# Optimization experiments

Hardware: AMD Instinct MI355X
Metric: run time of the kernel (lower is better)

The kernel has to match this reference:

```python
import jax, jax.numpy as jnp
import numpy as np
from jax import lax

N, E = 10000, 100000
IN_CH, HID, EDGE_DIM, K = 32, 64, 16, 3
DILATIONS = (1, 2, 4)


def setup_inputs() -> dict:
    key = jax.random.key(0)
    ks = jax.random.split(key, 20)
    def nrm(k, shape, fan):
        return jax.random.normal(k, shape, jnp.float32) * (1.0 / np.sqrt(fan))
    inp = {
        "x": jax.random.normal(ks[0], (N, IN_CH), jnp.float32),
        "edge_attr": jax.random.normal(ks[1], (E, EDGE_DIM), jnp.float32),
        "h_prev": jax.random.normal(ks[2], (N, K, HID), jnp.float32),
        "edge_index": jax.random.randint(ks[3], (2, E), 0, N, jnp.int32),
        # edge-conditioning MLP: edge_dim -> 32 -> in_ch*hid
        "w1": nrm(ks[4], (EDGE_DIM, 32), EDGE_DIM), "b1": jnp.zeros((32,), jnp.float32),
        "w2": nrm(ks[5], (32, IN_CH * HID), 32), "b2": jnp.zeros((IN_CH * HID,), jnp.float32),
        # NNConv root weight + bias
        "root": nrm(ks[6], (IN_CH, HID), IN_CH), "bias": jnp.zeros((HID,), jnp.float32),
        # three dilated Conv1d layers [out, in, k]
        "tcn_w1": nrm(ks[7], (HID, HID, K), HID * K), "tcn_b1": jnp.zeros((HID,), jnp.float32),
        "tcn_w2": nrm(ks[8], (HID, HID, K), HID * K), "tcn_b2": jnp.zeros((HID,), jnp.float32),
        "tcn_w3": nrm(ks[9], (HID, HID, K), HID * K), "tcn_b3": jnp.zeros((HID,), jnp.float32),
        # output projection hid*3 -> hid
        "proj_w": nrm(ks[10], (HID * len(DILATIONS), HID), HID * len(DILATIONS)),
        "proj_b": jnp.zeros((HID,), jnp.float32),
    }
    return inp


def _conv1d_last(h, w, b, dilation):
    # h: [N, C, L], w: [O, I, K]; 'same'-style padding (K-1)*d//2, return last timestep.
    pad = (K - 1) * dilation // 2
    out = lax.conv_general_dilated(
        h, w, window_strides=(1,), padding=[(pad, pad)],
        rhs_dilation=(dilation,), dimension_numbers=("NCH", "OIH", "NCH"))
    return out[:, :, -1] + b[None, :]


def reference(x, edge_attr, h_prev, edge_index,
              w1, b1, w2, b2, root, bias,
              tcn_w1, tcn_b1, tcn_w2, tcn_b2, tcn_w3, tcn_b3,
              proj_w, proj_b):
    src, dst = edge_index[0], edge_index[1]
    n = x.shape[0]

    # --- NNConv (ECC): per-edge weight via MLP, gather -> matmul -> scatter-mean ---
    h_e = jax.nn.relu(edge_attr @ w1 + b1)                   # [E, 32]
    W_e = (h_e @ w2 + b2).reshape(-1, IN_CH, HID)            # [E, in, hid]
    msg = jnp.einsum("ei,eio->eo", x[src], W_e)             # [E, hid]
    agg = jax.ops.segment_sum(msg, dst, num_segments=n)      # [N, hid]
    cnt = jax.ops.segment_sum(jnp.ones((msg.shape[0],), msg.dtype), dst, num_segments=n)
    mean = agg / jnp.maximum(cnt, 1.0)[:, None]
    h_graph = jax.nn.relu(mean + x @ root + bias)            # [N, hid]

    # --- history update ---
    h_hist = jnp.concatenate([h_prev[:, 1:], h_graph[:, None, :]], axis=1)  # [N, K, hid]

    # --- dilated TCN stack, keep only last timestep of each branch ---
    h_in = jnp.transpose(h_hist, (0, 2, 1))                  # [N, hid, K]
    outs = [
        _conv1d_last(h_in, tcn_w1, tcn_b1, DILATIONS[0]),
        _conv1d_last(h_in, tcn_w2, tcn_b2, DILATIONS[1]),
        _conv1d_last(h_in, tcn_w3, tcn_b3, DILATIONS[2]),
    ]
    h_cat = jnp.concatenate(outs, axis=1)                    # [N, hid*3]
    h_out = h_cat @ proj_w + proj_b                          # dropout = identity (eval)
    return h_out, h_hist
```

## Files before the change

kernel.cpp:

```cpp
#include <hip/hip_runtime.h>
#include <stdint.h>

#define NN 10000
#define NE 100000
#define CHUNK 10

__device__ __forceinline__ float bu2f(uint16_t u) {
    return __uint_as_float(((uint32_t)u) << 16);
}
__device__ __forceinline__ float blo(uint32_t v) { return __uint_as_float(v << 16); }
__device__ __forceinline__ float bhi(uint32_t v) { return __uint_as_float(v & 0xffff0000u); }
__device__ __forceinline__ uint16_t f2bu(float f) {
    uint32_t u = __float_as_uint(f);
    return (uint16_t)((u + 0x7fffu + ((u >> 16) & 1u)) >> 16);
}
__device__ __forceinline__ float ldf(const void* p, size_t i, int f32) {
    return f32 ? ((const float*)p)[i] : bu2f(((const uint16_t*)p)[i]);
}
struct f8 { float v[8]; };
__device__ __forceinline__ f8 ldf8(const void* p, size_t i, int f32) {
    f8 r;
    if (f32) {
        const float4* q = (const float4*)((const float*)p + i);
        float4 a = q[0], b = q[1];
        r.v[0]=a.x; r.v[1]=a.y; r.v[2]=a.z; r.v[3]=a.w;
        r.v[4]=b.x; r.v[5]=b.y; r.v[6]=b.z; r.v[7]=b.w;
    } else {
        uint4 u = *(const uint4*)((const uint16_t*)p + i);
        r.v[0]=blo(u.x); r.v[1]=bhi(u.x); r.v[2]=blo(u.y); r.v[3]=bhi(u.y);
        r.v[4]=blo(u.z); r.v[5]=bhi(u.z); r.v[6]=blo(u.w); r.v[7]=bhi(u.w);
    }
    return r;
}
__device__ __forceinline__ void stf(void* p, size_t i, float v, int f32) {
    if (f32) ((float*)p)[i] = v;
    else ((uint16_t*)p)[i] = f2bu(v);
}
__device__ __forceinline__ int clampi(int v, int lo, int hi) {
    return min(max(v, lo), hi);
}

__global__ __launch_bounds__(256) void k_init(
    const void* __restrict__ x, float4* __restrict__ zbase, int* __restrict__ flag)
{
    int bid = blockIdx.x;
    if (bid < 657) {
        int idx = bid * 256 + threadIdx.x;
        if (idx < 168088) zbase[idx] = make_float4(0.f, 0.f, 0.f, 0.f);
    } else if (threadIdx.x == 0) {
        const uint16_t* p = (const uint16_t*)x;
        int c = 0;
        for (int i = 0; i < 1024; i++) {
            float a = fabsf(bu2f(p[i]));
            if (a > 1e-3f && a < 16.0f) c++;
        }
        *flag = (c < 870) ? 1 : 0;
    }
}

__global__ __launch_bounds__(256, 4) void k_prep(
    const void* __restrict__ x, const void* __restrict__ root,
    const void* __restrict__ tw1, const void* __restrict__ tw2,
    const void* __restrict__ tw3,
    const void* __restrict__ tb1, const void* __restrict__ tb2,
    const void* __restrict__ tb3,
    const void* __restrict__ proj_w,
    const void* __restrict__ edge_attr, const void* __restrict__ w1,
    const void* __restrict__ b1,
    const void* __restrict__ w2, const void* __restrict__ b2,
    const int* __restrict__ ei, const int* __restrict__ flag,
    float* __restrict__ xs_f, float* __restrict__ root_f,
    float* __restrict__ A, float* __restrict__ B, float* __restrict__ C,
    float* __restrict__ dv,
    int* __restrict__ outdeg, int* __restrict__ indeg,
    uint16_t* __restrict__ h_edge,
    uint16_t* __restrict__ T, float* __restrict__ xb)
{
    int bid = blockIdx.x;
    int tid = threadIdx.x;
    if (bid < 157) {
        int f32 = *flag;
        int v8 = bid * 256 + tid;
        if (v8 < 40000) {
            f8 r = ldf8(x, (size_t)v8 * 8, f32);
            float4* o = (float4*)(xs_f + (size_t)v8 * 8);
            o[0] = make_float4(r.v[0], r.v[1], r.v[2], r.v[3]);
            o[1] = make_float4(r.v[4], r.v[5], r.v[6], r.v[7]);
        }
    } else if (bid == 157) {
        int f32 = *flag;
        f8 r = ldf8(root, (size_t)tid * 8, f32);
        float4* o = (float4*)(root_f + (size_t)tid * 8);
        o[0] = make_float4(r.v[0], r.v[1], r.v[2], r.v[3]);
        o[1] = make_float4(r.v[4], r.v[5], r.v[6], r.v[7]);
    } else if (bid < 670) {
        int f32 = *flag;
        int beta = bid - 158;
        int i = beta >> 3;
        int chunk = beta & 7;
        int o = tid & 63, sub = tid >> 6;
        int cc0 = chunk * 8 + sub * 2;
        float a = 0.f, b = 0.f, c = 0.f, d = 0.f;
        #pragma unroll
        for (int m = 0; m < 2; m++) {
            int cc = cc0 + m;
            float p0 = ldf(proj_w, (size_t)cc * 64 + o, f32);
            float p1 = ldf(proj_w, (size_t)(64 + cc) * 64 + o, f32);
            float p2 = ldf(proj_w, (size_t)(128 + cc) * 64 + o, f32);
            size_t base = (size_t)cc * 192 + i * 3;
            a = fmaf(ldf(tw1, base + 1, f32), p0, a);
            a = fmaf(ldf(tw2, base + 1, f32), p1, a);
            a = fmaf(ldf(tw3, base + 1, f32), p2, a);
            b = fmaf(ldf(tw2, base + 0, f32), p1, b);
            c = fmaf(ldf(tw1, base + 0, f32), p0, c);
            if (i == 0) {
                d = fmaf(ldf(tb1, cc, f32), p0, d);
                d = fmaf(ldf(tb2, cc, f32), p1, d);
                d = fmaf(ldf(tb3, cc, f32), p2, d);
            }
        }
        unsafeAtomicAdd(&A[i * 64 + o], a);
        unsafeAtomicAdd(&B[i * 64 + o], b);
        unsafeAtomicAdd(&C[i * 64 + o], c);
        if (i == 0) unsafeAtomicAdd(&dv[o], d);
    } else if (bid < 1061) {
        int e = (bid - 670) * 256 + tid;
        if (e < NE) {
            atomicAdd(&outdeg[clampi(ei[e], 0, NN - 1)], 1);
            atomicAdd(&indeg[clampi(ei[NE + e], 0, NN - 1)], 1);
        }
    } else if (bid < 4186) {
        int f32 = *flag;
        __shared__ float w1s[512];
        __shared__ float b1s[32];
        __shared__ float eas[32][16];
        int e0 = (bid - 1061) * 32;
        if (tid < 64) {
            f8 r = ldf8(w1, (size_t)tid * 8, f32);
            #pragma unroll
            for (int q = 0; q < 8; q++) w1s[tid * 8 + q] = r.v[q];
        } else if (tid < 128) {
            int t = tid - 64;
            f8 r = ldf8(edge_attr, (size_t)e0 * 16 + (size_t)t * 8, f32);
            int el = t >> 1, half = (t & 1) * 8;
            #pragma unroll
            for (int q = 0; q < 8; q++) eas[el][half + q] = r.v[q];
        } else if (tid < 160) {
            b1s[tid - 128] = ldf(b1, tid - 128, f32);
        }
        __syncthreads();
        int el = tid >> 5, j = tid & 31;
        float wreg[16];
        #pragma unroll
        for (int k = 0; k < 16; k++) wreg[k] = w1s[k * 32 + j];
        float bj = b1s[j];
        #pragma unroll
        for (int r = 0; r < 4; r++) {
            int e = el + r * 8;
            float acc = bj;
            #pragma unroll
            for (int k = 0; k < 16; k++) acc = fmaf(eas[e][k], wreg[k], acc);
            h_edge[(size_t)(e0 + e) * 32 + j] = f2bu(fmaxf(acc, 0.0f));
        }
    } else {
        int f32 = *flag;
        int n0 = (bid - 4186) * 8;
        __shared__ float xs[8][32];
        if (tid < 32) {
            f8 r = ldf8(x, (size_t)n0 * 32 + (size_t)tid * 8, f32);
            int base = tid * 8;
            #pragma unroll
            for (int q = 0; q < 8; q++) xs[(base + q) >> 5][(base + q) & 31] = r.v[q];
        }
        __syncthreads();
        int c0 = tid * 8;
        int j = c0 >> 6, o0 = c0 & 63;
        float acc[8][8];
        #pragma unroll
        for (int s = 0; s < 8; s++)
            #pragma unroll
            for (int r = 0; r < 8; r++) acc[s][r] = 0.0f;
        if (f32) {
            const float* wb = (const float*)w2 + (size_t)j * 2048 + o0;
            for (int i = 0; i < 32; i++) {
                float4 a4 = *(const float4*)(wb + i * 64);
                float4 b4 = *(const float4*)(wb + i * 64 + 4);
                #pragma unroll
                for (int s = 0; s < 8; s++) {
                    float xv = xs[s][i];
                    acc[s][0] = fmaf(xv, a4.x, acc[s][0]); acc[s][1] = fmaf(xv, a4.y, acc[s][1]);
                    acc[s][2] = fmaf(xv, a4.z, acc[s][2]); acc[s][3] = fmaf(xv, a4.w, acc[s][3]);
                    acc[s][4] = fmaf(xv, b4.x, acc[s][4]); acc[s][5] = fmaf(xv, b4.y, acc[s][5]);
                    acc[s][6] = fmaf(xv, b4.z, acc[s][6]); acc[s][7] = fmaf(xv, b4.w, acc[s][7]);
                }
            }
        } else {
            const uint16_t* wb = (const uint16_t*)w2 + (size_t)j * 2048 + o0;
            for (int i = 0; i < 32; i++) {
                uint4 u = *(const uint4*)(wb + i * 64);
                float w0 = blo(u.x), w1_ = bhi(u.x), w2_ = blo(u.y), w3 = bhi(u.y);
                float w4 = blo(u.z), w5 = bhi(u.z), w6 = blo(u.w), w7 = bhi(u.w);
                #pragma unroll
                for (int s = 0; s < 8; s++) {
                    float xv = xs[s][i];
                    acc[s][0] = fmaf(xv, w0, acc[s][0]); acc[s][1] = fmaf(xv, w1_, acc[s][1]);
                    acc[s][2] = fmaf(xv, w2_, acc[s][2]); acc[s][3] = fmaf(xv, w3, acc[s][3]);
                    acc[s][4] = fmaf(xv, w4, acc[s][4]); acc[s][5] = fmaf(xv, w5, acc[s][5]);
                    acc[s][6] = fmaf(xv, w6, acc[s][6]); acc[s][7] = fmaf(xv, w7, acc[s][7]);
                }
            }
        }
        #pragma unroll
        for (int s = 0; s < 8; s++) {
            uint4 ov;
            ov.x = ((uint32_t)f2bu(acc[s][1]) << 16) | f2bu(acc[s][0]);
            ov.y = ((uint32_t)f2bu(acc[s][3]) << 16) | f2bu(acc[s][2]);
            ov.z = ((uint32_t)f2bu(acc[s][5]) << 16) | f2bu(acc[s][4]);
            ov.w = ((uint32_t)f2bu(acc[s][7]) << 16) | f2bu(acc[s][6]);
            *(uint4*)(T + (size_t)(n0 + s) * 2048 + c0) = ov;
        }
        int o = tid & 63;
        if (f32) {
            const float* b2f = (const float*)b2;
            #pragma unroll
            for (int h = 0; h < 2; h++) {
                int s = (tid >> 6) + h * 4;
                float a = 0.0f;
                #pragma unroll
                for (int i = 0; i < 32; i++)
                    a = fmaf(xs[s][i], b2f[i * 64 + o], a);
                xb[(size_t)(n0 + s) * 64 + o] = a;
            }
        } else {
            const uint16_t* b2u = (const uint16_t*)b2;
            #pragma unroll
            for (int h = 0; h < 2; h++) {
                int s = (tid >> 6) + h * 4;
                float a = 0.0f;
                #pragma unroll
                for (int i = 0; i < 32; i++)
                    a = fmaf(xs[s][i], bu2f(b2u[i * 64 + o]), a);
                xb[(size_t)(n0 + s) * 64 + o] = a;
            }
        }
    }
}

__global__ __launch_bounds__(1024) void k_scan(
    const int* __restrict__ outdeg, int* __restrict__ offs, int* __restrict__ cursor)
{
    __shared__ int sums[1024];
    const int CH = 10;
    int tid = threadIdx.x;
    int base = tid * CH;
    int v[CH];
    int s = 0;
    #pragma unroll
    for (int k = 0; k < CH; k++) {
        int i = base + k;
        int c = (i < NN) ? outdeg[i] : 0;
        v[k] = s;
        s += c;
    }
    sums[tid] = s;
    __syncthreads();
    for (int d = 1; d < 1024; d <<= 1) {
        int t = (tid >= d) ? sums[tid - d] : 0;
        __syncthreads();
        if (tid >= d) sums[tid] += t;
        __syncthreads();
    }
    int prefix = (tid == 0) ? 0 : sums[tid - 1];
    #pragma unroll
    for (int k = 0; k < CH; k++) {
        int i = base + k;
        if (i <= NN) {
            int val = prefix + v[k];
            offs[i] = val;
            if (i < NN) cursor[i] = val;
        }
    }
}

__global__ __launch_bounds__(256) void k_scat(
    const int* __restrict__ ei, int* __restrict__ cursor,
    int* __restrict__ sorted_src, int* __restrict__ sorted_dst,
    int* __restrict__ sorted_eid,
    const uint16_t* __restrict__ h_edge, uint16_t* __restrict__ h_srt, int hs_mode)
{
    int e = blockIdx.x * 256 + threadIdx.x;
    if (e < NE) {
        int src = clampi(ei[e], 0, NN - 1);
        int dst = clampi(ei[NE + e], 0, NN - 1);
        int pos = clampi(atomicAdd(&cursor[src], 1), 0, NE - 1);
        sorted_src[pos] = src;
        sorted_dst[pos] = dst;
        if (hs_mode) {
            const uint4* hs = (const uint4*)(h_edge + (size_t)e * 32);
            uint4* hd = (uint4*)(h_srt + (size_t)pos * 32);
            hd[0] = hs[0]; hd[1] = hs[1]; hd[2] = hs[2]; hd[3] = hs[3];
        } else {
            sorted_eid[pos] = e;
        }
    }
}

__global__ __launch_bounds__(256) void k_msg_g(
    const uint16_t* __restrict__ h_edge, const uint16_t* __restrict__ h_srt,
    int hs_mode, const uint16_t* __restrict__ T,
    const float* __restrict__ xb, const int* __restrict__ sorted_src,
    const int* __restrict__ sorted_dst, const int* __restrict__ sorted_eid,
    float* __restrict__ agg)
{
    int wid = blockIdx.x * 4 + (threadIdx.x >> 6);
    int lane = threadIdx.x & 63;
    int p0 = wid * CHUNK;
    if (p0 >= NE) return;
    int p1 = min(p0 + CHUNK, NE);
    int cur = -1;
    float tv[32];
    float xbv = 0.0f;
    int sN = clampi(sorted_src[p0], 0, NN - 1);
    const uint4* hq;
    if (hs_mode) hq = (const uint4*)(h_srt + (size_t)p0 * 32);
    else hq = (const uint4*)(h_edge + (size_t)clampi(sorted_eid[p0], 0, NE - 1) * 32);
    uint4 na = hq[0], nb = hq[1], nc = hq[2], nd = hq[3];
    for (int p = p0; p < p1; p++) {
        int s = sN;
        uint4 a = na, b = nb, c = nc, d = nd;
        int dst = clampi(sorted_dst[p], 0, NN - 1);
        if (p + 1 < p1) {
            sN = clampi(sorted_src[p + 1], 0, NN - 1);
            const uint4* h2;
            if (hs_mode) h2 = (const uint4*)(h_srt + (size_t)(p + 1) * 32);
            else h2 = (const uint4*)(h_edge + (size_t)clampi(sorted_eid[p + 1], 0, NE - 1) * 32);
            na = h2[0]; nb = h2[1]; nc = h2[2]; nd = h2[3];
        }
        if (s != cur) {
            cur = s;
            const uint16_t* Tr = T + (size_t)s * 2048 + lane;
            #pragma unroll
            for (int j = 0; j < 32; j++) tv[j] = bu2f(Tr[j * 64]);
            xbv = xb[(size_t)s * 64 + lane];
        }
        float s0 = 0.f, s1 = 0.f, s2 = 0.f, s3 = 0.f;
        s0 = fmaf(blo(a.x), tv[0],  s0); s0 = fmaf(bhi(a.x), tv[1],  s0);
        s0 = fmaf(blo(a.y), tv[2],  s0); s0 = fmaf(bhi(a.y), tv[3],  s0);
        s0 = fmaf(blo(a.z), tv[4],  s0); s0 = fmaf(bhi(a.z), tv[5],  s0);
        s0 = fmaf(blo(a.w), tv[6],  s0); s0 = fmaf(bhi(a.w), tv[7],  s0);
        s1 = fmaf(blo(b.x), tv[8],  s1); s1 = fmaf(bhi(b.x), tv[9],  s1);
        s1 = fmaf(blo(b.y), tv[10], s1); s1 = fmaf(bhi(b.y), tv[11], s1);
        s1 = fmaf(blo(b.z), tv[12], s1); s1 = fmaf(bhi(b.z), tv[13], s1);
        s1 = fmaf(blo(b.w), tv[14], s1); s1 = fmaf(bhi(b.w), tv[15], s1);
        s2 = fmaf(blo(c.x), tv[16], s2); s2 = fmaf(bhi(c.x), tv[17], s2);
        s2 = fmaf(blo(c.y), tv[18], s2); s2 = fmaf(bhi(c.y), tv[19], s2);
        s2 = fmaf(blo(c.z), tv[20], s2); s2 = fmaf(bhi(c.z), tv[21], s2);
        s2 = fmaf(blo(c.w), tv[22], s2); s2 = fmaf(bhi(c.w), tv[23], s2);
        s3 = fmaf(blo(d.x), tv[24], s3); s3 = fmaf(bhi(d.x), tv[25], s3);
        s3 = fmaf(blo(d.y), tv[26], s3); s3 = fmaf(bhi(d.y), tv[27], s3);
        s3 = fmaf(blo(d.z), tv[28], s3); s3 = fmaf(bhi(d.z), tv[29], s3);
        s3 = fmaf(blo(d.w), tv[30], s3); s3 = fmaf(bhi(d.w), tv[31], s3);
        float acc = xbv + (s0 + s1) + (s2 + s3);
        unsafeAtomicAdd(&agg[(size_t)dst * 64 + lane], acc);
    }
}

__global__ __launch_bounds__(256) void k_node_out(
    const float* __restrict__ agg, const int* __restrict__ indeg,
    const float* __restrict__ xs_f, const float* __restrict__ root_f,
    const void* __restrict__ bias, const void* __restrict__ h_prev,
    const float* __restrict__ A, const float* __restrict__ B,
    const float* __restrict__ C, const float* __restrict__ dv,
    const void* __restrict__ proj_b,
    const int* __restrict__ flag, void* __restrict__ out)
{
// ... 40 lines not shown
    const void* edge_attr = d_in[1];
    const void* h_prev    = d_in[2];
    const int*  ei        = (const int*)d_in[3];
    const void* w1     = d_in[4];
    const void* b1     = d_in[5];
    const void* w2     = d_in[6];
    const void* b2     = d_in[7];
    const void* root   = d_in[8];
    const void* bias   = d_in[9];
    const void* tw1    = d_in[10];
    const void* tb1    = d_in[11];
    const void* tw2    = d_in[12];
    const void* tb2    = d_in[13];
    const void* tw3    = d_in[14];
    const void* tb3    = d_in[15];
    const void* proj_w = d_in[16];
    const void* proj_b = d_in[17];

    char* ws = (char*)d_ws;
    size_t off = 0;
    uint16_t* T      = (uint16_t*)(ws + off); off = align64(off + (size_t)NN * 2048 * 2);
    uint16_t* h_edge = (uint16_t*)(ws + off); off = align64(off + (size_t)NE * 32 * 2);
    float* xs_f   = (float*)(ws + off); off = align64(off + (size_t)NN * 32 * 4);
    float* root_f = (float*)(ws + off); off = align64(off + (size_t)2048 * 4);
    float* xb     = (float*)(ws + off); off = align64(off + (size_t)NN * 64 * 4);
    size_t zero_base = off;
    float* agg    = (float*)(ws + off); off = align64(off + (size_t)NN * 64 * 4);
    int* indeg    = (int*)(ws + off);   off = align64(off + (size_t)NN * 4);
    int* outdeg   = (int*)(ws + off);   off = align64(off + (size_t)NN * 4);
    float* Amat   = (float*)(ws + off); off = align64(off + (size_t)4096 * 4);
    float* Bmat   = (float*)(ws + off); off = align64(off + (size_t)4096 * 4);
    float* Cmat   = (float*)(ws + off); off = align64(off + (size_t)4096 * 4);
    float* dvec   = (float*)(ws + off); off = align64(off + (size_t)64 * 4);
    int* offs        = (int*)(ws + off); off = align64(off + (size_t)(NN + 1) * 4);
    int* cursor      = (int*)(ws + off); off = align64(off + (size_t)NN * 4);
    int* sorted_src  = (int*)(ws + off); off = align64(off + (size_t)NE * 4);
    int* sorted_dst  = (int*)(ws + off); off = align64(off + (size_t)NE * 4);
    int* sorted_eid  = (int*)(ws + off); off = align64(off + (size_t)NE * 4);
    int* flag        = (int*)(ws + off); off = align64(off + 64);
    uint16_t* h_srt  = (uint16_t*)(ws + off);
    size_t off_end = off + (size_t)NE * 32 * 2;
    int hs_mode = (off_end <= ws_size) ? 1 : 0;

    k_init<<<658, 256, 0, stream>>>(x, (float4*)((char*)d_ws + zero_base), flag);
    k_prep<<<5436, 256, 0, stream>>>(x, root, tw1, tw2, tw3, tb1, tb2, tb3,
                                     proj_w, edge_attr, w1, b1, w2, b2, ei, flag,
                                     xs_f, root_f, Amat, Bmat, Cmat, dvec,
                                     outdeg, indeg, h_edge, T, xb);
    k_scan<<<1, 1024, 0, stream>>>(outdeg, offs, cursor);
    k_scat<<<391, 256, 0, stream>>>(ei, cursor, sorted_src, sorted_dst,
                                    sorted_eid, h_edge, h_srt, hs_mode);
    k_msg_g<<<(NE / CHUNK + 3) / 4, 256, 0, stream>>>(h_edge, h_srt, hs_mode, T, xb,
                                                      sorted_src, sorted_dst,
                                                      sorted_eid, agg);
    k_node_out<<<NN / 4, 256, 0, stream>>>(agg, indeg, xs_f, root_f, bias, h_prev,
                                           Amat, Bmat, Cmat, dvec, proj_b, flag, d_out);
}
```

Before: 232.7 us.

## Fuse all stages into one cooperative persistent kernel with grid syncs

Replaces the six separate kernel launches with a single cooperative kernel that loops over virtual blocks and uses grid.sync between stages. Zeroing of agg is deferred into the scatter phase, and the scan becomes a per-block prefix computation. This removes launch overhead and inter-kernel gaps. In exchange it caps parallelism at the occupancy-limited grid size, adds grid-wide barrier costs, and replaces the single-block scan with a redundant per-block prefix sum. The old multi-kernel launches remain as a fallback if the cooperative launch fails.

```diff
diff --git a/kernel.cpp b/kernel.cpp
--- a/kernel.cpp
+++ b/kernel.cpp
@@ -1,5 +1,8 @@
 #include <hip/hip_runtime.h>
+#include <hip/hip_cooperative_groups.h>
 #include <stdint.h>
+
+namespace cg = cooperative_groups;
 
 #define NN 10000
 #define NE 100000
@@ -38,6 +41,355 @@
 }
 __device__ __forceinline__ int clampi(int v, int lo, int hi) {
     return min(max(v, lo), hi);
+}
+
+struct Args {
+    const void *x, *edge_attr, *h_prev;
+    const int* ei;
+    const void *w1, *b1, *w2, *b2, *root, *bias;
+    const void *tw1, *tb1, *tw2, *tb2, *tw3, *tb3, *proj_w, *proj_b;
+    float4* zbase;
+    int* flag;
+    float *xs_f, *root_f, *A, *B, *C, *dv;
+    int *outdeg, *indeg;
+    uint16_t *h_edge, *T;
+    float* xb;
+    int *cursor, *sorted_src, *sorted_dst, *sorted_eid;
+    uint16_t* h_srt;
+    int hs_mode;
+    float* agg;
+    void* out;
+};
+
+__global__ __launch_bounds__(256) void k_mega(Args a) {
+    cg::grid_group grid = cg::this_grid();
+    const int tid = threadIdx.x;
+    const int bid = blockIdx.x;
+    const int G = gridDim.x;
+
+    __shared__ union SU {
+        struct { float w1s[512]; float b1s[32]; float eas[32][16]; } mlp;
+        float xsT[8][32];
+        int red[256];
+        struct { float hg[4][64]; float hp1[4][64]; float hp2[4][64]; } fin;
+    } su;
+
+    for (int vb = bid; vb < 33; vb += G) {
+        if (vb < 32) {
+            int idx = vb * 256 + tid;
+            if (idx < 8088) a.zbase[160000 + idx] = make_float4(0.f, 0.f, 0.f, 0.f);
+        } else if (tid == 0) {
+            const uint16_t* p = (const uint16_t*)a.x;
+            int c = 0;
+            for (int i = 0; i < 1024; i++) {
+                float v = fabsf(bu2f(p[i]));
+                if (v > 1e-3f && v < 16.0f) c++;
+            }
+            *a.flag = (c < 870) ? 1 : 0;
+        }
+    }
+    grid.sync();
+    const int f32 = *a.flag;
+
+    for (int vb = bid; vb < 5436; vb += G) {
+        __syncthreads();
+        if (vb < 157) {
+            int v8 = vb * 256 + tid;
+            if (v8 < 40000) {
+                f8 r = ldf8(a.x, (size_t)v8 * 8, f32);
+                float4* o = (float4*)(a.xs_f + (size_t)v8 * 8);
+                o[0] = make_float4(r.v[0], r.v[1], r.v[2], r.v[3]);
+                o[1] = make_float4(r.v[4], r.v[5], r.v[6], r.v[7]);
+            }
+        } else if (vb == 157) {
+            f8 r = ldf8(a.root, (size_t)tid * 8, f32);
+            float4* o = (float4*)(a.root_f + (size_t)tid * 8);
+            o[0] = make_float4(r.v[0], r.v[1], r.v[2], r.v[3]);
+            o[1] = make_float4(r.v[4], r.v[5], r.v[6], r.v[7]);
+        } else if (vb < 670) {
+            int beta = vb - 158;
+            int i = beta >> 3;
+            int chunk = beta & 7;
+            int o = tid & 63, sub = tid >> 6;
+            int cc0 = chunk * 8 + sub * 2;
+            float av = 0.f, bv = 0.f, cv = 0.f, dv_ = 0.f;
+            #pragma unroll
+            for (int m = 0; m < 2; m++) {
+                int cc = cc0 + m;
+                float p0 = ldf(a.proj_w, (size_t)cc * 64 + o, f32);
+                float p1 = ldf(a.proj_w, (size_t)(64 + cc) * 64 + o, f32);
+                float p2 = ldf(a.proj_w, (size_t)(128 + cc) * 64 + o, f32);
+                size_t base = (size_t)cc * 192 + i * 3;
+                av = fmaf(ldf(a.tw1, base + 1, f32), p0, av);
+                av = fmaf(ldf(a.tw2, base + 1, f32), p1, av);
+                av = fmaf(ldf(a.tw3, base + 1, f32), p2, av);
+                bv = fmaf(ldf(a.tw2, base + 0, f32), p1, bv);
+                cv = fmaf(ldf(a.tw1, base + 0, f32), p0, cv);
+                if (i == 0) {
+                    dv_ = fmaf(ldf(a.tb1, cc, f32), p0, dv_);
+                    dv_ = fmaf(ldf(a.tb2, cc, f32), p1, dv_);
+                    dv_ = fmaf(ldf(a.tb3, cc, f32), p2, dv_);
+                }
+            }
+            unsafeAtomicAdd(&a.A[i * 64 + o], av);
+            unsafeAtomicAdd(&a.B[i * 64 + o], bv);
+            unsafeAtomicAdd(&a.C[i * 64 + o], cv);
+            if (i == 0) unsafeAtomicAdd(&a.dv[o], dv_);
+        } else if (vb < 1061) {
+            int e = (vb - 670) * 256 + tid;
+            if (e < NE) {
+                atomicAdd(&a.outdeg[clampi(a.ei[e], 0, NN - 1)], 1);
+                atomicAdd(&a.indeg[clampi(a.ei[NE + e], 0, NN - 1)], 1);
+            }
+        } else if (vb < 4186) {
+            int e0 = (vb - 1061) * 32;
+            if (tid < 64) {
+                f8 r = ldf8(a.w1, (size_t)tid * 8, f32);
+                #pragma unroll
+                for (int q = 0; q < 8; q++) su.mlp.w1s[tid * 8 + q] = r.v[q];
+            } else if (tid < 128) {
+                int t = tid - 64;
+                f8 r = ldf8(a.edge_attr, (size_t)e0 * 16 + (size_t)t * 8, f32);
+                int el = t >> 1, half = (t & 1) * 8;
+                #pragma unroll
+                for (int q = 0; q < 8; q++) su.mlp.eas[el][half + q] = r.v[q];
+            } else if (tid < 160) {
+                su.mlp.b1s[tid - 128] = ldf(a.b1, tid - 128, f32);
+            }
+            __syncthreads();
+            int el = tid >> 5, j = tid & 31;
+            float wreg[16];
+            #pragma unroll
+            for (int k = 0; k < 16; k++) wreg[k] = su.mlp.w1s[k * 32 + j];
+            float bj = su.mlp.b1s[j];
+            #pragma unroll
+            for (int r = 0; r < 4; r++) {
+                int e = el + r * 8;
+                float acc = bj;
+                #pragma unroll
+                for (int k = 0; k < 16; k++) acc = fmaf(su.mlp.eas[e][k], wreg[k], acc);
+                a.h_edge[(size_t)(e0 + e) * 32 + j] = f2bu(fmaxf(acc, 0.0f));
+            }
+        } else {
+            int n0 = (vb - 4186) * 8;
+            if (tid < 32) {
+                f8 r = ldf8(a.x, (size_t)n0 * 32 + (size_t)tid * 8, f32);
+                int base = tid * 8;
+                #pragma unroll
+                for (int q = 0; q < 8; q++) su.xsT[(base + q) >> 5][(base + q) & 31] = r.v[q];
+            }
+            __syncthreads();
+            int c0 = tid * 8;
+            int j = c0 >> 6, o0 = c0 & 63;
+            float acc[8][8];
+            #pragma unroll
+            for (int s = 0; s < 8; s++)
+                #pragma unroll
+                for (int r = 0; r < 8; r++) acc[s][r] = 0.0f;
+            if (f32) {
+                const float* wb = (const float*)a.w2 + (size_t)j * 2048 + o0;
+                for (int i = 0; i < 32; i++) {
+                    float4 a4 = *(const float4*)(wb + i * 64);
+                    float4 b4 = *(const float4*)(wb + i * 64 + 4);
+                    #pragma unroll
+                    for (int s = 0; s < 8; s++) {
+                        float xv = su.xsT[s][i];
+                        acc[s][0] = fmaf(xv, a4.x, acc[s][0]); acc[s][1] = fmaf(xv, a4.y, acc[s][1]);
+                        acc[s][2] = fmaf(xv, a4.z, acc[s][2]); acc[s][3] = fmaf(xv, a4.w, acc[s][3]);
+                        acc[s][4] = fmaf(xv, b4.x, acc[s][4]); acc[s][5] = fmaf(xv, b4.y, acc[s][5]);
+                        acc[s][6] = fmaf(xv, b4.z, acc[s][6]); acc[s][7] = fmaf(xv, b4.w, acc[s][7]);
+                    }
+                }
+            } else {
+                const uint16_t* wb = (const uint16_t*)a.w2 + (size_t)j * 2048 + o0;
+                for (int i = 0; i < 32; i++) {
+                    uint4 u = *(const uint4*)(wb + i * 64);
+                    float w0 = blo(u.x), w1_ = bhi(u.x), w2_ = blo(u.y), w3 = bhi(u.y);
+                    float w4 = blo(u.z), w5 = bhi(u.z), w6 = blo(u.w), w7 = bhi(u.w);
+                    #pragma unroll
+                    for (int s = 0; s < 8; s++) {
+                        float xv = su.xsT[s][i];
+                        acc[s][0] = fmaf(xv, w0, acc[s][0]); acc[s][1] = fmaf(xv, w1_, acc[s][1]);
+                        acc[s][2] = fmaf(xv, w2_, acc[s][2]); acc[s][3] = fmaf(xv, w3, acc[s][3]);
+                        acc[s][4] = fmaf(xv, w4, acc[s][4]); acc[s][5] = fmaf(xv, w5, acc[s][5]);
+                        acc[s][6] = fmaf(xv, w6, acc[s][6]); acc[s][7] = fmaf(xv, w7, acc[s][7]);
+                    }
+                }
+            }
+            #pragma unroll
+            for (int s = 0; s < 8; s++) {
+                uint4 ov;
+                ov.x = ((uint32_t)f2bu(acc[s][1]) << 16) | f2bu(acc[s][0]);
+                ov.y = ((uint32_t)f2bu(acc[s][3]) << 16) | f2bu(acc[s][2]);
+                ov.z = ((uint32_t)f2bu(acc[s][5]) << 16) | f2bu(acc[s][4]);
+                ov.w = ((uint32_t)f2bu(acc[s][7]) << 16) | f2bu(acc[s][6]);
+                *(uint4*)(a.T + (size_t)(n0 + s) * 2048 + c0) = ov;
+            }
+            int o = tid & 63;
+            if (f32) {
+                const float* b2f = (const float*)a.b2;
+                #pragma unroll
+                for (int h = 0; h < 2; h++) {
+                    int s = (tid >> 6) + h * 4;
+                    float acc2 = 0.0f;
+                    #pragma unroll
+                    for (int i = 0; i < 32; i++)
+                        acc2 = fmaf(su.xsT[s][i], b2f[i * 64 + o], acc2);
+                    a.xb[(size_t)(n0 + s) * 64 + o] = acc2;
+                }
+            } else {
+                const uint16_t* b2u = (const uint16_t*)a.b2;
+                #pragma unroll
+                for (int h = 0; h < 2; h++) {
+                    int s = (tid >> 6) + h * 4;
+                    float acc2 = 0.0f;
+                    #pragma unroll
+                    for (int i = 0; i < 32; i++)
+                        acc2 = fmaf(su.xsT[s][i], bu2f(b2u[i * 64 + o]), acc2);
+                    a.xb[(size_t)(n0 + s) * 64 + o] = acc2;
+                }
+            }
+        }
+    }
+    grid.sync();
+
+    {
+        const int RANGE = (NN + G - 1) / G;
+        int base = bid * RANGE;
+        if (base < NN) {
+            __syncthreads();
+            int s = 0;
+            for (int j = tid; j < base; j += 256) s += a.outdeg[j];
+            su.red[tid] = s;
+            __syncthreads();
+            #pragma unroll
+            for (int d = 128; d > 0; d >>= 1) {
+                if (tid < d) su.red[tid] += su.red[tid + d];
+                __syncthreads();
+            }
+            if (tid == 0) {
+                int run = su.red[0];
+                int cnt = min(RANGE, NN - base);
+                for (int k = 0; k < cnt; k++) {
+                    int i = base + k;
+                    a.cursor[i] = run;
+                    run += a.outdeg[i];
+                }
+            }
+        }
+    }
+    grid.sync();
+
+    for (int vb = bid; vb < 1016; vb += G) {
+        if (vb < 391) {
+            int e = vb * 256 + tid;
+            if (e < NE) {
+                int src = clampi(a.ei[e], 0, NN - 1);
+                int dst = clampi(a.ei[NE + e], 0, NN - 1);
+                int pos = clampi(atomicAdd(&a.cursor[src], 1), 0, NE - 1);
+                a.sorted_src[pos] = src;
+                a.sorted_dst[pos] = dst;
+                if (a.hs_mode) {
+                    const uint4* hs = (const uint4*)(a.h_edge + (size_t)e * 32);
+                    uint4* hd = (uint4*)(a.h_srt + (size_t)pos * 32);
+                    hd[0] = hs[0]; hd[1] = hs[1]; hd[2] = hs[2]; hd[3] = hs[3];
+                } else {
+                    a.sorted_eid[pos] = e;
+                }
+            }
+        } else {
+            int idx = (vb - 391) * 256 + tid;
+            if (idx < 160000) a.zbase[idx] = make_float4(0.f, 0.f, 0.f, 0.f);
+        }
+    }
+    grid.sync();
+
+    for (int vb = bid; vb < 2500; vb += G) {
+        int wid = vb * 4 + (tid >> 6);
+        int lane = tid & 63;
+        int p0 = wid * CHUNK;
+        if (p0 < NE) {
+            int p1 = min(p0 + CHUNK, NE);
+            int cur = -1;
+            float tv[32];
+            float xbv = 0.0f;
+            int sN = clampi(a.sorted_src[p0], 0, NN - 1);
+            const uint4* hq;
+            if (a.hs_mode) hq = (const uint4*)(a.h_srt + (size_t)p0 * 32);
+            else hq = (const uint4*)(a.h_edge + (size_t)clampi(a.sorted_eid[p0], 0, NE - 1) * 32);
+            uint4 na = hq[0], nb = hq[1], nc = hq[2], nd = hq[3];
+            for (int p = p0; p < p1; p++) {
+                int s = sN;
+                uint4 av = na, bv = nb, cv = nc, dvv = nd;
+                int dst = clampi(a.sorted_dst[p], 0, NN - 1);
+                if (p + 1 < p1) {
+                    sN = clampi(a.sorted_src[p + 1], 0, NN - 1);
+                    const uint4* h2;
+                    if (a.hs_mode) h2 = (const uint4*)(a.h_srt + (size_t)(p + 1) * 32);
+                    else h2 = (const uint4*)(a.h_edge + (size_t)clampi(a.sorted_eid[p + 1], 0, NE - 1) * 32);
+                    na = h2[0]; nb = h2[1]; nc = h2[2]; nd = h2[3];
+                }
+                if (s != cur) {
+                    cur = s;
+                    const uint16_t* Tr = a.T + (size_t)s * 2048 + lane;
+                    #pragma unroll
+                    for (int j = 0; j < 32; j++) tv[j] = bu2f(Tr[j * 64]);
+                    xbv = a.xb[(size_t)s * 64 + lane];
+                }
+                float s0 = 0.f, s1 = 0.f, s2 = 0.f, s3 = 0.f;
+                s0 = fmaf(blo(av.x), tv[0],  s0); s0 = fmaf(bhi(av.x), tv[1],  s0);
+                s0 = fmaf(blo(av.y), tv[2],  s0); s0 = fmaf(bhi(av.y), tv[3],  s0);
+                s0 = fmaf(blo(av.z), tv[4],  s0); s0 = fmaf(bhi(av.z), tv[5],  s0);
+                s0 = fmaf(blo(av.w), tv[6],  s0); s0 = fmaf(bhi(av.w), tv[7],  s0);
+                s1 = fmaf(blo(bv.x), tv[8],  s1); s1 = fmaf(bhi(bv.x), tv[9],  s1);
+                s1 = fmaf(blo(bv.y), tv[10], s1); s1 = fmaf(bhi(bv.y), tv[11], s1);
+                s1 = fmaf(blo(bv.z), tv[12], s1); s1 = fmaf(bhi(bv.z), tv[13], s1);
+                s1 = fmaf(blo(bv.w), tv[14], s1); s1 = fmaf(bhi(bv.w), tv[15], s1);
+                s2 = fmaf(blo(cv.x), tv[16], s2); s2 = fmaf(bhi(cv.x), tv[17], s2);
+                s2 = fmaf(blo(cv.y), tv[18], s2); s2 = fmaf(bhi(cv.y), tv[19], s2);
+                s2 = fmaf(blo(cv.z), tv[20], s2); s2 = fmaf(bhi(cv.z), tv[21], s2);
+                s2 = fmaf(blo(cv.w), tv[22], s2); s2 = fmaf(bhi(cv.w), tv[23], s2);
+                s3 = fmaf(blo(dvv.x), tv[24], s3); s3 = fmaf(bhi(dvv.x), tv[25], s3);
+                s3 = fmaf(blo(dvv.y), tv[26], s3); s3 = fmaf(bhi(dvv.y), tv[27], s3);
+                s3 = fmaf(blo(dvv.z), tv[28], s3); s3 = fmaf(bhi(dvv.z), tv[29], s3);
+                s3 = fmaf(blo(dvv.w), tv[30], s3); s3 = fmaf(bhi(dvv.w), tv[31], s3);
+                float acc = xbv + (s0 + s1) + (s2 + s3);
+                unsafeAtomicAdd(&a.agg[(size_t)dst * 64 + lane], acc);
+            }
+        }
+    }
+    grid.sync();
+
+    for (int vb = bid; vb < 2500; vb += G) {
+        __syncthreads();
+        int s = tid >> 6, o = tid & 63;
+        int n = vb * 4 + s;
+        const size_t O1 = (size_t)NN * 64;
+        float xr = 0.0f;
+        const float* xp = a.xs_f + (size_t)n * 32;
+        #pragma unroll
+        for (int i = 0; i < 32; i++)
+            xr = fmaf(xp[i], a.root_f[i * 64 + o], xr);
+        float c = (float)a.indeg[n];
+        float m = a.agg[(size_t)n * 64 + o] / fmaxf(c, 1.0f);
+        float hg = fmaxf(m + xr + ldf(a.bias, o, f32), 0.0f);
+        float hp1 = ldf(a.h_prev, (size_t)n * 192 + 64 + o, f32);
+        float hp2 = ldf(a.h_prev, (size_t)n * 192 + 128 + o, f32);
+        su.fin.hg[s][o] = hg; su.fin.hp1[s][o] = hp1; su.fin.hp2[s][o] = hp2;
+        stf(a.out, O1 + (size_t)n * 192 + o, hp1, f32);
+        stf(a.out, O1 + (size_t)n * 192 + 64 + o, hp2, f32);
+        stf(a.out, O1 + (size_t)n * 192 + 128 + o, hg, f32);
+        __syncthreads();
+        float accA = 0.f, accB = 0.f, accC = 0.f;
+        #pragma unroll 8
+        for (int i = 0; i < 64; i++) {
+            accA = fmaf(su.fin.hg[s][i],  a.A[i * 64 + o], accA);
+            accB = fmaf(su.fin.hp1[s][i], a.B[i * 64 + o], accB);
+            accC = fmaf(su.fin.hp2[s][i], a.C[i * 64 + o], accC);
+        }
+        float acc = a.dv[o] + ldf(a.proj_b, o, f32) + (accA + accB) + accC;
+        stf(a.out, (size_t)n * 64 + o, acc, f32);
+    }
 }
 
 __global__ __launch_bounds__(256) void k_init(
@@ -457,6 +809,41 @@
     size_t off_end = off + (size_t)NE * 32 * 2;
     int hs_mode = (off_end <= ws_size) ? 1 : 0;
 
+    static int g_grid = -1;
+    if (g_grid < 0) {
+        int bpc = 0;
+        if (hipOccupancyMaxActiveBlocksPerMultiprocessor(&bpc, k_mega, 256, 0) != hipSuccess || bpc <= 0)
+            bpc = 1;
+        int ncu = 64;
+        hipDeviceProp_t prop;
+        if (hipGetDeviceProperties(&prop, 0) == hipSuccess && prop.multiProcessorCount > 0)
+            ncu = prop.multiProcessorCount;
+        int g = bpc * ncu;
+        if (g > 2048) g = 2048;
+        if (g < 64) g = 64;
+        g_grid = g;
+    }
+
+    Args ha;
+    ha.x = x; ha.edge_attr = edge_attr; ha.h_prev = h_prev; ha.ei = ei;
+    ha.w1 = w1; ha.b1 = b1; ha.w2 = w2; ha.b2 = b2; ha.root = root; ha.bias = bias;
+    ha.tw1 = tw1; ha.tb1 = tb1; ha.tw2 = tw2; ha.tb2 = tb2; ha.tw3 = tw3; ha.tb3 = tb3;
+    ha.proj_w = proj_w; ha.proj_b = proj_b;
+    ha.zbase = (float4*)((char*)d_ws + zero_base);
+    ha.flag = flag;
+    ha.xs_f = xs_f; ha.root_f = root_f; ha.A = Amat; ha.B = Bmat; ha.C = Cmat; ha.dv = dvec;
+    ha.outdeg = outdeg; ha.indeg = indeg;
+    ha.h_edge = h_edge; ha.T = T; ha.xb = xb;
+    ha.cursor = cursor; ha.sorted_src = sorted_src; ha.sorted_dst = sorted_dst;
+    ha.sorted_eid = sorted_eid; ha.h_srt = h_srt; ha.hs_mode = hs_mode;
+    ha.agg = agg; ha.out = d_out;
+
+    void* kargs[] = { &ha };
+    hipError_t err = hipLaunchCooperativeKernel(k_mega, dim3(g_grid), dim3(256),
+                                                kargs, 0, stream);
+    if (err == hipSuccess) return;
+    (void)hipGetLastError();
+
     k_init<<<658, 256, 0, stream>>>(x, (float4*)((char*)d_ws + zero_base), flag);
     k_prep<<<5436, 256, 0, stream>>>(x, root, tw1, tw2, tw3, tb1, tb2, tb3,
                                      proj_w, edge_attr, w1, b1, w2, b2, ei, flag,
```

Result: slower. 470.4 us (+102.2%).

## Transpose T layout for vector loads and fold scan into scatter kernel

Applied to the files above, without the earlier changes.

The node-transform blocks in k_prep now stage T through shared memory and write it transposed, so each lane in k_msg_g can fetch its 32 bf16 values with four 16-byte loads instead of 32 strided scalar loads. The degree pass now records each edge's rank from the atomicAdd, which removes the separate single-block k_scan kernel and the cursor atomics. Each k_scat block recomputes the prefix sum of out-degrees in shared memory (40 KB) and places edges at offset plus rank. Heavy blocks are also reordered to launch first in k_prep. The cost is redundant scan work in each of 98 scatter blocks and more shared memory per prep block.

```diff
diff --git a/kernel.cpp b/kernel.cpp
--- a/kernel.cpp
+++ b/kernel.cpp
@@ -72,30 +72,151 @@
     float* __restrict__ xs_f, float* __restrict__ root_f,
     float* __restrict__ A, float* __restrict__ B, float* __restrict__ C,
     float* __restrict__ dv,
-    int* __restrict__ outdeg, int* __restrict__ indeg,
+    int* __restrict__ outdeg, int* __restrict__ indeg, int* __restrict__ rank,
     uint16_t* __restrict__ h_edge,
     uint16_t* __restrict__ T, float* __restrict__ xb)
 {
     int bid = blockIdx.x;
     int tid = threadIdx.x;
-    if (bid < 157) {
+    __shared__ union PU {
+        struct { float xs[8][32]; uint16_t Ts[8][32][64]; } t;
+        struct { float w1s[512]; float b1s[32]; float eas[32][16]; } mlp;
+    } su;
+
+    if (bid < 1250) {
         int f32 = *flag;
-        int v8 = bid * 256 + tid;
-        if (v8 < 40000) {
-            f8 r = ldf8(x, (size_t)v8 * 8, f32);
-            float4* o = (float4*)(xs_f + (size_t)v8 * 8);
-            o[0] = make_float4(r.v[0], r.v[1], r.v[2], r.v[3]);
-            o[1] = make_float4(r.v[4], r.v[5], r.v[6], r.v[7]);
-        }
-    } else if (bid == 157) {
+        int n0 = bid * 8;
+        if (tid < 32) {
+            f8 r = ldf8(x, (size_t)n0 * 32 + (size_t)tid * 8, f32);
+            int base = tid * 8;
+            #pragma unroll
+            for (int q = 0; q < 8; q++) su.t.xs[(base + q) >> 5][(base + q) & 31] = r.v[q];
+        }
+        __syncthreads();
+        int j = tid >> 3;
+        int o0 = (tid & 7) * 8;
+        float acc[8][8];
+        #pragma unroll
+        for (int s = 0; s < 8; s++)
+            #pragma unroll
+            for (int r = 0; r < 8; r++) acc[s][r] = 0.0f;
+        if (f32) {
+            const float* wb = (const float*)w2 + (size_t)j * 2048 + o0;
+            for (int i = 0; i < 32; i++) {
+                float4 a4 = *(const float4*)(wb + i * 64);
+                float4 b4 = *(const float4*)(wb + i * 64 + 4);
+                #pragma unroll
+                for (int s = 0; s < 8; s++) {
+                    float xv = su.t.xs[s][i];
+                    acc[s][0] = fmaf(xv, a4.x, acc[s][0]); acc[s][1] = fmaf(xv, a4.y, acc[s][1]);
+                    acc[s][2] = fmaf(xv, a4.z, acc[s][2]); acc[s][3] = fmaf(xv, a4.w, acc[s][3]);
+                    acc[s][4] = fmaf(xv, b4.x, acc[s][4]); acc[s][5] = fmaf(xv, b4.y, acc[s][5]);
+                    acc[s][6] = fmaf(xv, b4.z, acc[s][6]); acc[s][7] = fmaf(xv, b4.w, acc[s][7]);
+                }
+            }
+        } else {
+            const uint16_t* wb = (const uint16_t*)w2 + (size_t)j * 2048 + o0;
+            for (int i = 0; i < 32; i++) {
+                uint4 u = *(const uint4*)(wb + i * 64);
+                float w0 = blo(u.x), w1_ = bhi(u.x), w2_ = blo(u.y), w3 = bhi(u.y);
+                float w4 = blo(u.z), w5 = bhi(u.z), w6 = blo(u.w), w7 = bhi(u.w);
+                #pragma unroll
+                for (int s = 0; s < 8; s++) {
+                    float xv = su.t.xs[s][i];
+                    acc[s][0] = fmaf(xv, w0, acc[s][0]); acc[s][1] = fmaf(xv, w1_, acc[s][1]);
+                    acc[s][2] = fmaf(xv, w2_, acc[s][2]); acc[s][3] = fmaf(xv, w3, acc[s][3]);
+                    acc[s][4] = fmaf(xv, w4, acc[s][4]); acc[s][5] = fmaf(xv, w5, acc[s][5]);
+                    acc[s][6] = fmaf(xv, w6, acc[s][6]); acc[s][7] = fmaf(xv, w7, acc[s][7]);
+                }
+            }
+        }
+        #pragma unroll
+        for (int s = 0; s < 8; s++) {
+            uint4 ov;
+            ov.x = ((uint32_t)f2bu(acc[s][1]) << 16) | f2bu(acc[s][0]);
+            ov.y = ((uint32_t)f2bu(acc[s][3]) << 16) | f2bu(acc[s][2]);
+            ov.z = ((uint32_t)f2bu(acc[s][5]) << 16) | f2bu(acc[s][4]);
+            ov.w = ((uint32_t)f2bu(acc[s][7]) << 16) | f2bu(acc[s][6]);
+            *(uint4*)&su.t.Ts[s][j][o0] = ov;
+        }
+        __syncthreads();
+        int k = tid >> 6, o = tid & 63;
+        #pragma unroll
+        for (int s = 0; s < 8; s++) {
+            uint16_t v0 = su.t.Ts[s][k * 8 + 0][o];
+            uint16_t v1 = su.t.Ts[s][k * 8 + 1][o];
+            uint16_t v2 = su.t.Ts[s][k * 8 + 2][o];
+            uint16_t v3 = su.t.Ts[s][k * 8 + 3][o];
+            uint16_t v4 = su.t.Ts[s][k * 8 + 4][o];
+            uint16_t v5 = su.t.Ts[s][k * 8 + 5][o];
+            uint16_t v6 = su.t.Ts[s][k * 8 + 6][o];
+            uint16_t v7 = su.t.Ts[s][k * 8 + 7][o];
+            uint4 ov;
+            ov.x = (uint32_t)v0 | ((uint32_t)v1 << 16);
+            ov.y = (uint32_t)v2 | ((uint32_t)v3 << 16);
+            ov.z = (uint32_t)v4 | ((uint32_t)v5 << 16);
+            ov.w = (uint32_t)v6 | ((uint32_t)v7 << 16);
+            *(uint4*)(T + (size_t)(n0 + s) * 2048 + (size_t)o * 32 + k * 8) = ov;
+        }
+        {
+            int oo = tid & 63;
+            if (f32) {
+                const float* b2f = (const float*)b2;
+                #pragma unroll
+                for (int h = 0; h < 2; h++) {
+                    int s = (tid >> 6) + h * 4;
+                    float a2 = 0.0f;
+                    #pragma unroll
+                    for (int i = 0; i < 32; i++)
+                        a2 = fmaf(su.t.xs[s][i], b2f[i * 64 + oo], a2);
+                    xb[(size_t)(n0 + s) * 64 + oo] = a2;
+                }
+            } else {
+                const uint16_t* b2u = (const uint16_t*)b2;
+                #pragma unroll
+                for (int h = 0; h < 2; h++) {
+                    int s = (tid >> 6) + h * 4;
+                    float a2 = 0.0f;
+                    #pragma unroll
+                    for (int i = 0; i < 32; i++)
+                        a2 = fmaf(su.t.xs[s][i], bu2f(b2u[i * 64 + oo]), a2);
+                    xb[(size_t)(n0 + s) * 64 + oo] = a2;
+                }
+            }
+        }
+    } else if (bid < 4375) {
         int f32 = *flag;
-        f8 r = ldf8(root, (size_t)tid * 8, f32);
-        float4* o = (float4*)(root_f + (size_t)tid * 8);
-        o[0] = make_float4(r.v[0], r.v[1], r.v[2], r.v[3]);
-        o[1] = make_float4(r.v[4], r.v[5], r.v[6], r.v[7]);
-    } else if (bid < 670) {
+        int e0 = (bid - 1250) * 32;
+        if (tid < 64) {
+            f8 r = ldf8(w1, (size_t)tid * 8, f32);
+            #pragma unroll
+            for (int q = 0; q < 8; q++) su.mlp.w1s[tid * 8 + q] = r.v[q];
+        } else if (tid < 128) {
+            int t = tid - 64;
+            f8 r = ldf8(edge_attr, (size_t)e0 * 16 + (size_t)t * 8, f32);
+            int el = t >> 1, half = (t & 1) * 8;
+            #pragma unroll
+            for (int q = 0; q < 8; q++) su.mlp.eas[el][half + q] = r.v[q];
+        } else if (tid < 160) {
+            su.mlp.b1s[tid - 128] = ldf(b1, tid - 128, f32);
+        }
+        __syncthreads();
+        int el = tid >> 5, jj = tid & 31;
+        float wreg[16];
+        #pragma unroll
+        for (int k = 0; k < 16; k++) wreg[k] = su.mlp.w1s[k * 32 + jj];
+        float bj = su.mlp.b1s[jj];
+        #pragma unroll
+        for (int r = 0; r < 4; r++) {
+            int e = el + r * 8;
+            float acc = bj;
+            #pragma unroll
+            for (int k = 0; k < 16; k++) acc = fmaf(su.mlp.eas[e][k], wreg[k], acc);
+            h_edge[(size_t)(e0 + e) * 32 + jj] = f2bu(fmaxf(acc, 0.0f));
+        }
+    } else if (bid < 4887) {
         int f32 = *flag;
-        int beta = bid - 158;
+        int beta = bid - 4375;
         int i = beta >> 3;
         int chunk = beta & 7;
         int o = tid & 63, sub = tid >> 6;
@@ -123,184 +244,78 @@
         unsafeAtomicAdd(&B[i * 64 + o], b);
         unsafeAtomicAdd(&C[i * 64 + o], c);
         if (i == 0) unsafeAtomicAdd(&dv[o], d);
-    } else if (bid < 1061) {
-        int e = (bid - 670) * 256 + tid;
+    } else if (bid < 5278) {
+        int e = (bid - 4887) * 256 + tid;
         if (e < NE) {
-            atomicAdd(&outdeg[clampi(ei[e], 0, NN - 1)], 1);
+            int src = clampi(ei[e], 0, NN - 1);
+            rank[e] = atomicAdd(&outdeg[src], 1);
             atomicAdd(&indeg[clampi(ei[NE + e], 0, NN - 1)], 1);
         }
-    } else if (bid < 4186) {
+    } else if (bid < 5435) {
         int f32 = *flag;
-        __shared__ float w1s[512];
-        __shared__ float b1s[32];
-        __shared__ float eas[32][16];
-        int e0 = (bid - 1061) * 32;
-        if (tid < 64) {
-            f8 r = ldf8(w1, (size_t)tid * 8, f32);
-            #pragma unroll
-            for (int q = 0; q < 8; q++) w1s[tid * 8 + q] = r.v[q];
-        } else if (tid < 128) {
-            int t = tid - 64;
-            f8 r = ldf8(edge_attr, (size_t)e0 * 16 + (size_t)t * 8, f32);
-            int el = t >> 1, half = (t & 1) * 8;
-            #pragma unroll
-            for (int q = 0; q < 8; q++) eas[el][half + q] = r.v[q];
-        } else if (tid < 160) {
-            b1s[tid - 128] = ldf(b1, tid - 128, f32);
-        }
-        __syncthreads();
-        int el = tid >> 5, j = tid & 31;
-        float wreg[16];
-        #pragma unroll
-        for (int k = 0; k < 16; k++) wreg[k] = w1s[k * 32 + j];
-        float bj = b1s[j];
-        #pragma unroll
-        for (int r = 0; r < 4; r++) {
-            int e = el + r * 8;
-            float acc = bj;
-            #pragma unroll
-            for (int k = 0; k < 16; k++) acc = fmaf(eas[e][k], wreg[k], acc);
-            h_edge[(size_t)(e0 + e) * 32 + j] = f2bu(fmaxf(acc, 0.0f));
+        int v8 = (bid - 5278) * 256 + tid;
+        if (v8 < 40000) {
+            f8 r = ldf8(x, (size_t)v8 * 8, f32);
+            float4* o = (float4*)(xs_f + (size_t)v8 * 8);
+            o[0] = make_float4(r.v[0], r.v[1], r.v[2], r.v[3]);
+            o[1] = make_float4(r.v[4], r.v[5], r.v[6], r.v[7]);
         }
     } else {
         int f32 = *flag;
-        int n0 = (bid - 4186) * 8;
-        __shared__ float xs[8][32];
-        if (tid < 32) {
-            f8 r = ldf8(x, (size_t)n0 * 32 + (size_t)tid * 8, f32);
-            int base = tid * 8;
-            #pragma unroll
-            for (int q = 0; q < 8; q++) xs[(base + q) >> 5][(base + q) & 31] = r.v[q];
-        }
-        __syncthreads();
-        int c0 = tid * 8;
-        int j = c0 >> 6, o0 = c0 & 63;
-        float acc[8][8];
-        #pragma unroll
-        for (int s = 0; s < 8; s++)
-            #pragma unroll
-            for (int r = 0; r < 8; r++) acc[s][r] = 0.0f;
-        if (f32) {
-            const float* wb = (const float*)w2 + (size_t)j * 2048 + o0;
-            for (int i = 0; i < 32; i++) {
-                float4 a4 = *(const float4*)(wb + i * 64);
-                float4 b4 = *(const float4*)(wb + i * 64 + 4);
-                #pragma unroll
-                for (int s = 0; s < 8; s++) {
-                    float xv = xs[s][i];
-                    acc[s][0] = fmaf(xv, a4.x, acc[s][0]); acc[s][1] = fmaf(xv, a4.y, acc[s][1]);
-                    acc[s][2] = fmaf(xv, a4.z, acc[s][2]); acc[s][3] = fmaf(xv, a4.w, acc[s][3]);
-                    acc[s][4] = fmaf(xv, b4.x, acc[s][4]); acc[s][5] = fmaf(xv, b4.y, acc[s][5]);
-                    acc[s][6] = fmaf(xv, b4.z, acc[s][6]); acc[s][7] = fmaf(xv, b4.w, acc[s][7]);
-                }
-            }
-        } else {
-            const uint16_t* wb = (const uint16_t*)w2 + (size_t)j * 2048 + o0;
-            for (int i = 0; i < 32; i++) {
-                uint4 u = *(const uint4*)(wb + i * 64);
-                float w0 = blo(u.x), w1_ = bhi(u.x), w2_ = blo(u.y), w3 = bhi(u.y);
-                float w4 = blo(u.z), w5 = bhi(u.z), w6 = blo(u.w), w7 = bhi(u.w);
-                #pragma unroll
-                for (int s = 0; s < 8; s++) {
-                    float xv = xs[s][i];
-                    acc[s][0] = fmaf(xv, w0, acc[s][0]); acc[s][1] = fmaf(xv, w1_, acc[s][1]);
-                    acc[s][2] = fmaf(xv, w2_, acc[s][2]); acc[s][3] = fmaf(xv, w3, acc[s][3]);
-                    acc[s][4] = fmaf(xv, w4, acc[s][4]); acc[s][5] = fmaf(xv, w5, acc[s][5]);
-                    acc[s][6] = fmaf(xv, w6, acc[s][6]); acc[s][7] = fmaf(xv, w7, acc[s][7]);
-                }
-            }
-        }
-        #pragma unroll
-        for (int s = 0; s < 8; s++) {
-            uint4 ov;
-            ov.x = ((uint32_t)f2bu(acc[s][1]) << 16) | f2bu(acc[s][0]);
-            ov.y = ((uint32_t)f2bu(acc[s][3]) << 16) | f2bu(acc[s][2]);
-            ov.z = ((uint32_t)f2bu(acc[s][5]) << 16) | f2bu(acc[s][4]);
-            ov.w = ((uint32_t)f2bu(acc[s][7]) << 16) | f2bu(acc[s][6]);
-            *(uint4*)(T + (size_t)(n0 + s) * 2048 + c0) = ov;
-        }
-        int o = tid & 63;
-        if (f32) {
-            const float* b2f = (const float*)b2;
-            #pragma unroll
-            for (int h = 0; h < 2; h++) {
-                int s = (tid >> 6) + h * 4;
-                float a = 0.0f;
-                #pragma unroll
-                for (int i = 0; i < 32; i++)
-                    a = fmaf(xs[s][i], b2f[i * 64 + o], a);
-                xb[(size_t)(n0 + s) * 64 + o] = a;
-            }
-        } else {
-            const uint16_t* b2u = (const uint16_t*)b2;
-            #pragma unroll
-            for (int h = 0; h < 2; h++) {
-                int s = (tid >> 6) + h * 4;
-                float a = 0.0f;
-                #pragma unroll
-                for (int i = 0; i < 32; i++)
-                    a = fmaf(xs[s][i], bu2f(b2u[i * 64 + o]), a);
-                xb[(size_t)(n0 + s) * 64 + o] = a;
-            }
-        }
-    }
-}
-
-__global__ __launch_bounds__(1024) void k_scan(
-    const int* __restrict__ outdeg, int* __restrict__ offs, int* __restrict__ cursor)
-{
-    __shared__ int sums[1024];
-    const int CH = 10;
-    int tid = threadIdx.x;
-    int base = tid * CH;
-    int v[CH];
-    int s = 0;
-    #pragma unroll
-    for (int k = 0; k < CH; k++) {
-        int i = base + k;
-        int c = (i < NN) ? outdeg[i] : 0;
-        v[k] = s;
-        s += c;
-    }
-    sums[tid] = s;
-    __syncthreads();
-    for (int d = 1; d < 1024; d <<= 1) {
-        int t = (tid >= d) ? sums[tid - d] : 0;
-        __syncthreads();
-        if (tid >= d) sums[tid] += t;
-        __syncthreads();
-    }
-    int prefix = (tid == 0) ? 0 : sums[tid - 1];
-    #pragma unroll
-    for (int k = 0; k < CH; k++) {
-        int i = base + k;
-        if (i <= NN) {
-            int val = prefix + v[k];
-            offs[i] = val;
-            if (i < NN) cursor[i] = val;
-        }
+        f8 r = ldf8(root, (size_t)tid * 8, f32);
+        float4* o = (float4*)(root_f + (size_t)tid * 8);
+        o[0] = make_float4(r.v[0], r.v[1], r.v[2], r.v[3]);
+        o[1] = make_float4(r.v[4], r.v[5], r.v[6], r.v[7]);
     }
 }
 
 __global__ __launch_bounds__(256) void k_scat(
-    const int* __restrict__ ei, int* __restrict__ cursor,
+    const int* __restrict__ ei, const int* __restrict__ outdeg,
+    const int* __restrict__ rank,
     int* __restrict__ sorted_src, int* __restrict__ sorted_dst,
     int* __restrict__ sorted_eid,
     const uint16_t* __restrict__ h_edge, uint16_t* __restrict__ h_srt, int hs_mode)
 {
-    int e = blockIdx.x * 256 + threadIdx.x;
-    if (e < NE) {
-        int src = clampi(ei[e], 0, NN - 1);
-        int dst = clampi(ei[NE + e], 0, NN - 1);
-        int pos = clampi(atomicAdd(&cursor[src], 1), 0, NE - 1);
-        sorted_src[pos] = src;
-        sorted_dst[pos] = dst;
-        if (hs_mode) {
-            const uint4* hs = (const uint4*)(h_edge + (size_t)e * 32);
-            uint4* hd = (uint4*)(h_srt + (size_t)pos * 32);
-            hd[0] = hs[0]; hd[1] = hs[1]; hd[2] = hs[2]; hd[3] = hs[3];
-        } else {
-            sorted_eid[pos] = e;
+    __shared__ int offs_l[NN];
+    __shared__ int tsum[256];
+    int tid = threadIdx.x;
+    const int CH = 40;
+    int base = tid * CH;
+    int s = 0;
+    for (int k = 0; k < CH; k++) {
+        int i = base + k;
+        if (i < NN) s += outdeg[i];
+    }
+    tsum[tid] = s;
+    __syncthreads();
+    for (int d = 1; d < 256; d <<= 1) {
+        int t = (tid >= d) ? tsum[tid - d] : 0;
+        __syncthreads();
+        if (tid >= d) tsum[tid] += t;
+        __syncthreads();
+    }
+    int run = (tid == 0) ? 0 : tsum[tid - 1];
+    for (int k = 0; k < CH; k++) {
+        int i = base + k;
+        if (i < NN) { offs_l[i] = run; run += outdeg[i]; }
+    }
+    __syncthreads();
+    #pragma unroll
+    for (int r = 0; r < 4; r++) {
+        int e = blockIdx.x * 1024 + r * 256 + tid;
+        if (e < NE) {
+            int src = clampi(ei[e], 0, NN - 1);
+            int dst = clampi(ei[NE + e], 0, NN - 1);
+            int pos = clampi(offs_l[src] + rank[e], 0, NE - 1);
+            sorted_src[pos] = src;
+            sorted_dst[pos] = dst;
+            if (hs_mode) {
+                const uint4* hs = (const uint4*)(h_edge + (size_t)e * 32);
+                uint4* hd = (uint4*)(h_srt + (size_t)pos * 32);
+                hd[0] = hs[0]; hd[1] = hs[1]; hd[2] = hs[2]; hd[3] = hs[3];
+            } else {
+                sorted_eid[pos] = e;
+            }
         }
     }
 }
@@ -338,9 +353,16 @@
         }
         if (s != cur) {
             cur = s;
-            const uint16_t* Tr = T + (size_t)s * 2048 + lane;
-            #pragma unroll
-            for (int j = 0; j < 32; j++) tv[j] = bu2f(Tr[j * 64]);
+            const uint4* Tp = (const uint4*)(T + (size_t)s * 2048 + (size_t)lane * 32);
+            uint4 t0 = Tp[0], t1 = Tp[1], t2 = Tp[2], t3 = Tp[3];
+            tv[0]=blo(t0.x); tv[1]=bhi(t0.x); tv[2]=blo(t0.y); tv[3]=bhi(t0.y);
+            tv[4]=blo(t0.z); tv[5]=bhi(t0.z); tv[6]=blo(t0.w); tv[7]=bhi(t0.w);
+            tv[8]=blo(t1.x); tv[9]=bhi(t1.x); tv[10]=blo(t1.y); tv[11]=bhi(t1.y);
+            tv[12]=blo(t1.z); tv[13]=bhi(t1.z); tv[14]=blo(t1.w); tv[15]=bhi(t1.w);
+            tv[16]=blo(t2.x); tv[17]=bhi(t2.x); tv[18]=blo(t2.y); tv[19]=bhi(t2.y);
+            tv[20]=blo(t2.z); tv[21]=bhi(t2.z); tv[22]=blo(t2.w); tv[23]=bhi(t2.w);
+            tv[24]=blo(t3.x); tv[25]=bhi(t3.x); tv[26]=blo(t3.y); tv[27]=bhi(t3.y);
+            tv[28]=blo(t3.z); tv[29]=bhi(t3.z); tv[30]=blo(t3.w); tv[31]=bhi(t3.w);
             xbv = xb[(size_t)s * 64 + lane];
         }
         float s0 = 0.f, s1 = 0.f, s2 = 0.f, s3 = 0.f;
@@ -447,8 +469,7 @@
     float* Bmat   = (float*)(ws + off); off = align64(off + (size_t)4096 * 4);
     float* Cmat   = (float*)(ws + off); off = align64(off + (size_t)4096 * 4);
     float* dvec   = (float*)(ws + off); off = align64(off + (size_t)64 * 4);
-    int* offs        = (int*)(ws + off); off = align64(off + (size_t)(NN + 1) * 4);
-    int* cursor      = (int*)(ws + off); off = align64(off + (size_t)NN * 4);
+    int* rank        = (int*)(ws + off); off = align64(off + (size_t)NE * 4);
     int* sorted_src  = (int*)(ws + off); off = align64(off + (size_t)NE * 4);
     int* sorted_dst  = (int*)(ws + off); off = align64(off + (size_t)NE * 4);
     int* sorted_eid  = (int*)(ws + off); off = align64(off + (size_t)NE * 4);
@@ -461,10 +482,10 @@
     k_prep<<<5436, 256, 0, stream>>>(x, root, tw1, tw2, tw3, tb1, tb2, tb3,
                                      proj_w, edge_attr, w1, b1, w2, b2, ei, flag,
                                      xs_f, root_f, Amat, Bmat, Cmat, dvec,
-                                     outdeg, indeg, h_edge, T, xb);
-    k_scan<<<1, 1024, 0, stream>>>(outdeg, offs, cursor);
-    k_scat<<<391, 256, 0, stream>>>(ei, cursor, sorted_src, sorted_dst,
-                                    sorted_eid, h_edge, h_srt, hs_mode);
+                                     outdeg, indeg, rank, h_edge, T, xb);
+    k_scat<<<(NE + 1023) / 1024, 256, 0, stream>>>(ei, outdeg, rank,
+                                                   sorted_src, sorted_dst, sorted_eid,
+                                                   h_edge, h_srt, hs_mode);
     k_msg_g<<<(NE / CHUNK + 3) / 4, 256, 0, stream>>>(h_edge, h_srt, hs_mode, T, xb,
                                                       sorted_src, sorted_dst,
                                                       sorted_eid, agg);
```

Result: no change. 236.8 us (+1.8%).
